# Optimization experiments

Hardware: AMD Instinct MI355X
Metric: run time of the kernel (lower is better)

The kernel has to match this reference:

```python
import jax, jax.numpy as jnp
import numpy as np

B, N, M, C = 8, 76725, 32, 12  # N = 9 anchors x (80^2+40^2+20^2+10^2+5^2) for a 640x640 image, P3-P7
IMG = 640.0


def setup_inputs() -> dict:
    key = jax.random.key(0)
    ks = jax.random.split(key, 7)
    # logits biased toward prior_prob~0.01 like the head's bias init
    cls_logits = jax.random.normal(ks[0], (B, N, C), jnp.float32) - 4.0
    box_deltas = 0.1 * jax.random.normal(ks[1], (B, N, 4), jnp.float32)
    # plausible anchors: random centers in image, sizes 16..256
    a_xy = jax.random.uniform(ks[2], (N, 2), jnp.float32) * IMG
    a_wh = 16.0 + jax.random.uniform(ks[3], (N, 2), jnp.float32) * 240.0
    anchors = jnp.concatenate([a_xy - 0.5 * a_wh, a_xy + 0.5 * a_wh], axis=-1)
    # padded ground truth: M boxes per image, all valid
    g_xy = jax.random.uniform(ks[4], (B, M, 2), jnp.float32) * (IMG - 96.0)
    g_wh = 16.0 + jax.random.uniform(ks[5], (B, M, 2), jnp.float32) * 80.0
    gt_boxes = jnp.concatenate([g_xy, g_xy + g_wh], axis=-1)
    gt_labels = jax.random.randint(ks[6], (B, M), 0, C)
    gt_valid = jnp.ones((B, M), dtype=bool)
    return {"cls_logits": cls_logits, "box_deltas": box_deltas, "anchors": anchors,
            "gt_boxes": gt_boxes, "gt_labels": gt_labels, "gt_valid": gt_valid}


def _box_iou(anchors, gt_boxes):
    # anchors [N,4], gt_boxes [B,M,4] -> [B,N,M]
    ax1, ay1, ax2, ay2 = (anchors[:, i] for i in range(4))
    gx1, gy1, gx2, gy2 = (gt_boxes[..., i] for i in range(4))
    iw = jnp.clip(jnp.minimum(ax2[None, :, None], gx2[:, None, :])
                  - jnp.maximum(ax1[None, :, None], gx1[:, None, :]), 0.0)
    ih = jnp.clip(jnp.minimum(ay2[None, :, None], gy2[:, None, :])
                  - jnp.maximum(ay1[None, :, None], gy1[:, None, :]), 0.0)
    inter = iw * ih
    area_a = (ax2 - ax1) * (ay2 - ay1)            # [N]
    area_g = (gx2 - gx1) * (gy2 - gy1)            # [B,M]
    union = area_a[None, :, None] + area_g[:, None, :] - inter
    return inter / union


def _encode_boxes(anchors, matched):
    aw = anchors[:, 2] - anchors[:, 0]
    ah = anchors[:, 3] - anchors[:, 1]
    acx = anchors[:, 0] + 0.5 * aw
    acy = anchors[:, 1] + 0.5 * ah
    gw = matched[..., 2] - matched[..., 0]
    gh = matched[..., 3] - matched[..., 1]
    gcx = matched[..., 0] + 0.5 * gw
    gcy = matched[..., 1] + 0.5 * gh
    return jnp.stack([(gcx - acx) / aw, (gcy - acy) / ah,
                      jnp.log(gw / aw), jnp.log(gh / ah)], axis=-1)


def reference(cls_logits, box_deltas, anchors, gt_boxes, gt_labels, gt_valid):
    # --- anchor assignment (box_iou + max over GT) ---
    ious = _box_iou(anchors, gt_boxes)                       # [B,N,M]
    ious = jnp.where(gt_valid[:, None, :], ious, -1.0)
    iou_max = ious.max(axis=-1)                              # [B,N]
    idx = ious.argmax(axis=-1)                               # [B,N]
    pos = iou_max >= 0.5
    valid = pos | (iou_max < 0.4)                            # non-ignore anchors
    matched = jnp.take_along_axis(
        gt_boxes, jnp.broadcast_to(idx[:, :, None], (B, N, 4)), axis=1)  # [B,N,4]
    mlab = jnp.take_along_axis(gt_labels, idx, axis=1)       # [B,N]
    f32 = cls_logits.dtype
    cls_t = jax.nn.one_hot(mlab, C, dtype=f32) * pos[..., None].astype(f32)
    # --- sigmoid focal loss (alpha=0.25, gamma=2), mean over non-ignored elements ---
    p = jax.nn.sigmoid(cls_logits)
    ce = -(cls_t * jax.nn.log_sigmoid(cls_logits)
           + (1.0 - cls_t) * jax.nn.log_sigmoid(-cls_logits))
    pt = cls_t * p + (1.0 - cls_t) * (1.0 - p)
    alpha_t = cls_t * 0.25 + (1.0 - cls_t) * 0.75
    focal = alpha_t * (1.0 - pt) ** 2 * ce                   # [B,N,C]
    vw = valid.astype(f32)
    cls_loss = jnp.sum(focal * vw[..., None]) / jnp.maximum(jnp.sum(vw) * C, 1.0)
    # --- smooth L1 (beta=1) on positives, mean over selected elements ---
    box_t = _encode_boxes(anchors, matched)                  # [B,N,4]
    d = jnp.abs(box_deltas - box_t)
    sl1 = jnp.where(d < 1.0, 0.5 * d * d, d - 0.5)
    pw = pos.astype(f32)
    box_loss = jnp.sum(sl1 * pw[..., None]) / jnp.maximum(jnp.sum(pw) * 4.0, 1.0)
    return cls_loss + box_loss
```

## Files before the change

kernel.cpp:

```cpp
#include <hip/hip_runtime.h>
#include <math.h>

#define NB 8
#define NA 76725
#define NM 32
#define NC 12
#define BLK 256
#define GX  128
#define NBLOCKS (GX * NB)
#define NSLOTS 64
#define QUOTA (NBLOCKS / NSLOTS)


__global__ __launch_bounds__(BLK) void retina_fused(
    const float* __restrict__ cls_logits,
    const float* __restrict__ box_deltas,
    const float* __restrict__ anchors,
    const float* __restrict__ gt_boxes,
    const int* __restrict__ gt_labels,
    char* __restrict__ ws,
    unsigned int* __restrict__ cnt2,
    float* __restrict__ out)
{
    __shared__ float4 s_gt[NM];
    __shared__ float  s_area[NM];
    __shared__ int    s_lab[NM];
    __shared__ int    s_islast;

    const int b   = blockIdx.y;
    const int tid = threadIdx.x;

    if (tid < NM) {
        float4 g = ((const float4*)gt_boxes)[b * NM + tid];
        s_gt[tid]   = g;
        s_area[tid] = (g.z - g.x) * (g.w - g.y);
        s_lab[tid]  = gt_labels[b * NM + tid];
    }
    __syncthreads();

    float fsum = 0.0f;
    float ssum = 0.0f;
    int   vcnt = 0;
    int   pcnt = 0;

    for (int n0 = blockIdx.x * BLK; n0 < NA; n0 += GX * BLK) {
        const int n = n0 + tid;
        if (n >= NA) break;

        const float4 a = ((const float4*)anchors)[n];
        const float4* cl = (const float4*)(cls_logits + ((size_t)b * NA + n) * NC);
        const float4 c0 = cl[0], c1 = cl[1], c2 = cl[2];

        const float area_a = (a.z - a.x) * (a.w - a.y);

        float b_inter, b_uni;
        int   bidx = 0;
        {
            const float4 g = s_gt[0];
            const float iw = fmaxf(fminf(a.z, g.z) - fmaxf(a.x, g.x), 0.0f);
            const float ih = fmaxf(fminf(a.w, g.w) - fmaxf(a.y, g.y), 0.0f);
            b_inter = iw * ih;
            b_uni   = (area_a + s_area[0]) - b_inter;
        }
        #pragma unroll
        for (int m = 1; m < NM; ++m) {
            const float4 g = s_gt[m];
            const float iw = fmaxf(fminf(a.z, g.z) - fmaxf(a.x, g.x), 0.0f);
            const float ih = fmaxf(fminf(a.w, g.w) - fmaxf(a.y, g.y), 0.0f);
            const float inter = iw * ih;
            const float uni   = (area_a + s_area[m]) - inter;
            const bool gt = inter * b_uni > b_inter * uni;
            b_inter = gt ? inter : b_inter;
            b_uni   = gt ? uni   : b_uni;
            bidx    = gt ? m     : bidx;
        }

        const bool pos   = (b_inter >= 0.5f * b_uni);
        const bool valid = pos || (b_inter < 0.4f * b_uni);
        vcnt += valid ? 1 : 0;
        pcnt += pos ? 1 : 0;

        if (valid) {
            const int lab = pos ? s_lab[bidx] : -1;
            float x[NC];
            x[0]=c0.x; x[1]=c0.y; x[2]=c0.z; x[3]=c0.w;
            x[4]=c1.x; x[5]=c1.y; x[6]=c1.z; x[7]=c1.w;
            x[8]=c2.x; x[9]=c2.y; x[10]=c2.z; x[11]=c2.w;
            #pragma unroll
            for (int c = 0; c < NC; ++c) {
                const float xx = x[c];
                const float ax = fabsf(xx);
                const float e  = __expf(-ax);
                const float t  = 1.0f + e;
                const float l1pe = __logf(t);
                const float u  = __builtin_amdgcn_rcpf(t);
                const float v  = e * u;
                const bool xpos = (xx >= 0.0f);
                const float sp_mx = l1pe + fmaxf(-xx, 0.0f);
                const float sp_px = l1pe + fmaxf(xx, 0.0f);
                const bool tgt = (c == lab);
                const float q = tgt ? (xpos ? v : u) : (xpos ? u : v);
                const float s = tgt ? sp_mx : sp_px;
                const float al = tgt ? 0.25f : 0.75f;
                fsum += al * q * q * s;
            }
        }

        if (pos) {
            const float4 g = s_gt[bidx];
            const float aw  = a.z - a.x;
            const float ah  = a.w - a.y;
            const float r_aw = __builtin_amdgcn_rcpf(aw);
            const float r_ah = __builtin_amdgcn_rcpf(ah);
            const float acx = a.x + 0.5f * aw;
            const float acy = a.y + 0.5f * ah;
            const float gw  = g.z - g.x;
            const float gh  = g.w - g.y;
            const float gcx = g.x + 0.5f * gw;
            const float gcy = g.y + 0.5f * gh;
            const float t0 = (gcx - acx) * r_aw;
            const float t1 = (gcy - acy) * r_ah;
            const float t2 = __logf(gw * r_aw);
            const float t3 = __logf(gh * r_ah);
            const float4 d4 =
                ((const float4*)box_deltas)[(size_t)b * NA + n];
            float d;
            d = fabsf(d4.x - t0); ssum += (d < 1.0f) ? 0.5f * d * d : d - 0.5f;
            d = fabsf(d4.y - t1); ssum += (d < 1.0f) ? 0.5f * d * d : d - 0.5f;
            d = fabsf(d4.z - t2); ssum += (d < 1.0f) ? 0.5f * d * d : d - 0.5f;
            d = fabsf(d4.w - t3); ssum += (d < 1.0f) ? 0.5f * d * d : d - 0.5f;
        }
    }

    float4 v = make_float4(fsum, ssum, (float)vcnt, (float)pcnt);
    #pragma unroll
    for (int off = 32; off > 0; off >>= 1) {
        v.x += __shfl_down(v.x, off);
        v.y += __shfl_down(v.y, off);
        v.z += __shfl_down(v.z, off);
        v.w += __shfl_down(v.w, off);
    }
    __shared__ float4 s_red[BLK / 64];
    const int wave = tid >> 6;
    const int lane = tid & 63;
    if (lane == 0) s_red[wave] = v;
    __syncthreads();

    if (tid == 0) {
        float4 t = s_red[0];
        #pragma unroll
        for (int w = 1; w < BLK / 64; ++w) {
            t.x += s_red[w].x; t.y += s_red[w].y;
            t.z += s_red[w].z; t.w += s_red[w].w;
        }
        const int flat = blockIdx.y * GX + blockIdx.x;
        const int slot = flat & (NSLOTS - 1);
        double* acc = (double*)(ws + (size_t)slot * 64);
        atomicAdd(&acc[0], (double)t.x);
        atomicAdd(&acc[1], (double)t.y);
        atomicAdd(&acc[2], (double)t.z);
        atomicAdd(&acc[3], (double)t.w);
        __threadfence();
        unsigned int* slot_cnt = (unsigned int*)(ws + (size_t)slot * 64 + 32);
        const unsigned int old = atomicAdd(slot_cnt, 1u);
        int islast = 0;
        if (old == QUOTA - 1) {
            __threadfence();
            const unsigned int o2 = atomicAdd(cnt2, 1u);
            islast = (o2 == NSLOTS - 1) ? 1 : 0;
        }
        s_islast = islast;
    }
    __syncthreads();

    if (s_islast) {
        __threadfence();
        __shared__ double s_acc[NSLOTS][4];
        if (tid < NSLOTS) {
            const double* acc = (const double*)(ws + (size_t)tid * 64);
            #pragma unroll
            for (int j = 0; j < 4; ++j)
                s_acc[tid][j] = __hip_atomic_load(&acc[j], __ATOMIC_RELAXED,
                                                  __HIP_MEMORY_SCOPE_AGENT);
        }
        __syncthreads();
        if (tid == 0) {
            double fs = 0.0, ss = 0.0, vc = 0.0, pc = 0.0;
            for (int k = 0; k < NSLOTS; ++k) {
                fs += s_acc[k][0]; ss += s_acc[k][1];
                vc += s_acc[k][2]; pc += s_acc[k][3];
            }
            const double cls_loss = fs / fmax(vc * (double)NC, 1.0);
            const double box_loss = ss / fmax(pc * 4.0, 1.0);
            out[0] = (float)(cls_loss + box_loss);
        }
    }
}

extern "C" void kernel_launch(void* const* d_in, const int* in_sizes, int n_in,
                              void* d_out, int out_size, void* d_ws, size_t ws_size,
                              hipStream_t stream) {
    const float* cls_logits = (const float*)d_in[0];
    const float* box_deltas = (const float*)d_in[1];
    const float* anchors    = (const float*)d_in[2];
    const float* gt_boxes   = (const float*)d_in[3];
    const int*   gt_labels  = (const int*)d_in[4];
    float* out = (float*)d_out;

    char* ws = (char*)d_ws;
    unsigned int* cnt2 = (unsigned int*)(ws + (size_t)NSLOTS * 64);

    hipMemsetAsync(d_ws, 0, (size_t)NSLOTS * 64 + 4, stream);
    dim3 grid(GX, NB);
    retina_fused<<<grid, BLK, 0, stream>>>(
        cls_logits, box_deltas, anchors, gt_boxes, gt_labels,
        ws, cnt2, out);
}
```

Measured before the change: 124.8 us.

## Compute focal loss unconditionally and split IoU argmax into parallel groups

The focal loss for all 12 classes is now computed without a branch, treating every class as a negative. For positive anchors, the target class term is fixed up by reloading that single logit and swapping the negative term for the positive one. The 32-box IoU argmax is split into four independent chains of 8 and then merged in a small tree, which shortens the serial dependency chain and removes divergence around the valid branch. The cost is a transcendental pass on ignored anchors, an extra scattered global load for positives, and tie-breaking and rounding that may differ slightly from before.

```diff
diff --git a/kernel.cpp b/kernel.cpp
--- a/kernel.cpp
+++ b/kernel.cpp
@@ -53,60 +53,91 @@
 
         const float area_a = (a.z - a.x) * (a.w - a.y);
 
-        float b_inter, b_uni;
-        int   bidx = 0;
-        {
-            const float4 g = s_gt[0];
-            const float iw = fmaxf(fminf(a.z, g.z) - fmaxf(a.x, g.x), 0.0f);
-            const float ih = fmaxf(fminf(a.w, g.w) - fmaxf(a.y, g.y), 0.0f);
-            b_inter = iw * ih;
-            b_uni   = (area_a + s_area[0]) - b_inter;
-        }
+        float x[NC];
+        x[0]=c0.x; x[1]=c0.y; x[2]=c0.z; x[3]=c0.w;
+        x[4]=c1.x; x[5]=c1.y; x[6]=c1.z; x[7]=c1.w;
+        x[8]=c2.x; x[9]=c2.y; x[10]=c2.z; x[11]=c2.w;
+        float fall = 0.0f;
         #pragma unroll
-        for (int m = 1; m < NM; ++m) {
-            const float4 g = s_gt[m];
-            const float iw = fmaxf(fminf(a.z, g.z) - fmaxf(a.x, g.x), 0.0f);
-            const float ih = fmaxf(fminf(a.w, g.w) - fmaxf(a.y, g.y), 0.0f);
-            const float inter = iw * ih;
-            const float uni   = (area_a + s_area[m]) - inter;
-            const bool gt = inter * b_uni > b_inter * uni;
-            b_inter = gt ? inter : b_inter;
-            b_uni   = gt ? uni   : b_uni;
-            bidx    = gt ? m     : bidx;
-        }
+        for (int c = 0; c < NC; ++c) {
+            const float xx = x[c];
+            const float ax = fabsf(xx);
+            const float e  = __expf(-ax);
+            const float t  = 1.0f + e;
+            const float l1pe = __logf(t);
+            const float u  = __builtin_amdgcn_rcpf(t);
+            const float pm = e * u;
+            const float p  = (xx >= 0.0f) ? u : pm;
+            const float sp = l1pe + fmaxf(xx, 0.0f);
+            fall += p * p * sp;
+        }
+
+        float gi[4], gu[4];
+        int   gx[4];
+        #pragma unroll
+        for (int grp = 0; grp < 4; ++grp) {
+            const int base = grp << 3;
+            float bi_, bu_;
+            int   bx_ = base;
+            {
+                const float4 g = s_gt[base];
+                const float iw = fmaxf(fminf(a.z, g.z) - fmaxf(a.x, g.x), 0.0f);
+                const float ih = fmaxf(fminf(a.w, g.w) - fmaxf(a.y, g.y), 0.0f);
+                bi_ = iw * ih;
+                bu_ = (area_a + s_area[base]) - bi_;
+            }
+            #pragma unroll
+            for (int j = 1; j < 8; ++j) {
+                const int m = base + j;
+                const float4 g = s_gt[m];
+                const float iw = fmaxf(fminf(a.z, g.z) - fmaxf(a.x, g.x), 0.0f);
+                const float ih = fmaxf(fminf(a.w, g.w) - fmaxf(a.y, g.y), 0.0f);
+                const float inter = iw * ih;
+                const float uni   = (area_a + s_area[m]) - inter;
+                const bool gt = inter * bu_ > bi_ * uni;
+                bi_ = gt ? inter : bi_;
+                bu_ = gt ? uni   : bu_;
+                bx_ = gt ? m     : bx_;
+            }
+            gi[grp] = bi_; gu[grp] = bu_; gx[grp] = bx_;
+        }
+        const bool m01 = gi[1] * gu[0] > gi[0] * gu[1];
+        const float i01 = m01 ? gi[1] : gi[0];
+        const float u01 = m01 ? gu[1] : gu[0];
+        const int   x01 = m01 ? gx[1] : gx[0];
+        const bool m23 = gi[3] * gu[2] > gi[2] * gu[3];
+        const float i23 = m23 ? gi[3] : gi[2];
+        const float u23 = m23 ? gu[3] : gu[2];
+        const int   x23 = m23 ? gx[3] : gx[2];
+        const bool mf = i23 * u01 > i01 * u23;
+        const float b_inter = mf ? i23 : i01;
+        const float b_uni   = mf ? u23 : u01;
+        const int   bidx    = mf ? x23 : x01;
 
         const bool pos   = (b_inter >= 0.5f * b_uni);
         const bool valid = pos || (b_inter < 0.4f * b_uni);
         vcnt += valid ? 1 : 0;
         pcnt += pos ? 1 : 0;
 
-        if (valid) {
-            const int lab = pos ? s_lab[bidx] : -1;
-            float x[NC];
-            x[0]=c0.x; x[1]=c0.y; x[2]=c0.z; x[3]=c0.w;
-            x[4]=c1.x; x[5]=c1.y; x[6]=c1.z; x[7]=c1.w;
-            x[8]=c2.x; x[9]=c2.y; x[10]=c2.z; x[11]=c2.w;
-            #pragma unroll
-            for (int c = 0; c < NC; ++c) {
-                const float xx = x[c];
-                const float ax = fabsf(xx);
-                const float e  = __expf(-ax);
-                const float t  = 1.0f + e;
-                const float l1pe = __logf(t);
-                const float u  = __builtin_amdgcn_rcpf(t);
-                const float v  = e * u;
-                const bool xpos = (xx >= 0.0f);
-                const float sp_mx = l1pe + fmaxf(-xx, 0.0f);
-                const float sp_px = l1pe + fmaxf(xx, 0.0f);
-                const bool tgt = (c == lab);
-                const float q = tgt ? (xpos ? v : u) : (xpos ? u : v);
-                const float s = tgt ? sp_mx : sp_px;
-                const float al = tgt ? 0.25f : 0.75f;
-                fsum += al * q * q * s;
-            }
-        }
+        fsum += valid ? 0.75f * fall : 0.0f;
 
         if (pos) {
+            const int lab = s_lab[bidx];
+            const float xl = cls_logits[((size_t)b * NA + n) * NC + lab];
+            const float ax = fabsf(xl);
+            const float e  = __expf(-ax);
+            const float t  = 1.0f + e;
+            const float l1pe = __logf(t);
+            const float u  = __builtin_amdgcn_rcpf(t);
+            const float pm = e * u;
+            const float p  = (xl >= 0.0f) ? u : pm;
+            const float omp = (xl >= 0.0f) ? pm : u;
+            const float sp_px = l1pe + fmaxf(xl, 0.0f);
+            const float sp_mx = l1pe + fmaxf(-xl, 0.0f);
+            const float tgt = 0.25f * omp * omp * sp_mx;
+            const float nt  = 0.75f * p * p * sp_px;
+            fsum += tgt - nt;
+
             const float4 g = s_gt[bidx];
             const float aw  = a.z - a.x;
             const float ah  = a.w - a.y;
```

New measurement: 126.0 us. About the same (+1.0%).

## Launch one block per anchor tile and compute focal loss as all-negative plus target correction

Applied to the files above, without the earlier changes.

Replaces the grid-stride loop with one 256-anchor tile per block (300 blocks per image, 60 accumulator slots), so each thread handles one anchor. The focal loss is now computed unconditionally for every class as if negative, and a single-class correction for the labelled class is added only on positive anchors. This removes the per-class target select and the divergent valid branch. The shared-memory GT staging and its barrier are dropped in favour of direct global reads, and the IoU thresholds are rewritten as cross-multiplied comparisons on intersection and area sum. The cost is a larger grid with more blocks doing atomics, plus an extra scattered logit load on positives.

```diff
diff --git a/kernel.cpp b/kernel.cpp
--- a/kernel.cpp
+++ b/kernel.cpp
@@ -6,9 +6,9 @@
 #define NM 32
 #define NC 12
 #define BLK 256
-#define GX  128
-#define NBLOCKS (GX * NB)
-#define NSLOTS 64
+#define NBLK_X ((NA + BLK - 1) / BLK)
+#define NBLOCKS (NBLK_X * NB)
+#define NSLOTS 60
 #define QUOTA (NBLOCKS / NSLOTS)
 
 
@@ -22,92 +22,94 @@
     unsigned int* __restrict__ cnt2,
     float* __restrict__ out)
 {
-    __shared__ float4 s_gt[NM];
-    __shared__ float  s_area[NM];
-    __shared__ int    s_lab[NM];
     __shared__ int    s_islast;
+    __shared__ float4 s_red[BLK / 64];
+    __shared__ double s_acc[NSLOTS][4];
 
     const int b   = blockIdx.y;
     const int tid = threadIdx.x;
-
-    if (tid < NM) {
-        float4 g = ((const float4*)gt_boxes)[b * NM + tid];
-        s_gt[tid]   = g;
-        s_area[tid] = (g.z - g.x) * (g.w - g.y);
-        s_lab[tid]  = gt_labels[b * NM + tid];
-    }
-    __syncthreads();
+    const int n   = blockIdx.x * BLK + tid;
+    const bool live = (n < NA);
+
+    const float4* __restrict__ gtb =
+        (const float4*)(gt_boxes + (size_t)b * NM * 4);
 
     float fsum = 0.0f;
     float ssum = 0.0f;
     int   vcnt = 0;
     int   pcnt = 0;
 
-    for (int n0 = blockIdx.x * BLK; n0 < NA; n0 += GX * BLK) {
-        const int n = n0 + tid;
-        if (n >= NA) break;
-
+    if (live) {
         const float4 a = ((const float4*)anchors)[n];
         const float4* cl = (const float4*)(cls_logits + ((size_t)b * NA + n) * NC);
         const float4 c0 = cl[0], c1 = cl[1], c2 = cl[2];
-
         const float area_a = (a.z - a.x) * (a.w - a.y);
 
-        float b_inter, b_uni;
+        float xs[NC];
+        xs[0]=c0.x; xs[1]=c0.y; xs[2]=c0.z; xs[3]=c0.w;
+        xs[4]=c1.x; xs[5]=c1.y; xs[6]=c1.z; xs[7]=c1.w;
+        xs[8]=c2.x; xs[9]=c2.y; xs[10]=c2.z; xs[11]=c2.w;
+        float fall = 0.0f;
+        #pragma unroll
+        for (int c = 0; c < NC; ++c) {
+            const float xx = xs[c];
+            const float ax = fabsf(xx);
+            const float e  = __expf(-ax);
+            const float t  = 1.0f + e;
+            const float l1pe = __logf(t);
+            const float u  = __builtin_amdgcn_rcpf(t);
+            const float pm = e * u;
+            const float p  = (xx >= 0.0f) ? u : pm;
+            const float sp = l1pe + fmaxf(xx, 0.0f);
+            fall += p * p * sp;
+        }
+
+        float b_i, b_S;
         int   bidx = 0;
         {
-            const float4 g = s_gt[0];
+            const float4 g = gtb[0];
             const float iw = fmaxf(fminf(a.z, g.z) - fmaxf(a.x, g.x), 0.0f);
             const float ih = fmaxf(fminf(a.w, g.w) - fmaxf(a.y, g.y), 0.0f);
-            b_inter = iw * ih;
-            b_uni   = (area_a + s_area[0]) - b_inter;
+            b_i = iw * ih;
+            b_S = area_a + (g.z - g.x) * (g.w - g.y);
         }
         #pragma unroll
         for (int m = 1; m < NM; ++m) {
-            const float4 g = s_gt[m];
+            const float4 g = gtb[m];
             const float iw = fmaxf(fminf(a.z, g.z) - fmaxf(a.x, g.x), 0.0f);
             const float ih = fmaxf(fminf(a.w, g.w) - fmaxf(a.y, g.y), 0.0f);
             const float inter = iw * ih;
-            const float uni   = (area_a + s_area[m]) - inter;
-            const bool gt = inter * b_uni > b_inter * uni;
-            b_inter = gt ? inter : b_inter;
-            b_uni   = gt ? uni   : b_uni;
-            bidx    = gt ? m     : bidx;
-        }
-
-        const bool pos   = (b_inter >= 0.5f * b_uni);
-        const bool valid = pos || (b_inter < 0.4f * b_uni);
-        vcnt += valid ? 1 : 0;
-        pcnt += pos ? 1 : 0;
-
-        if (valid) {
-            const int lab = pos ? s_lab[bidx] : -1;
-            float x[NC];
-            x[0]=c0.x; x[1]=c0.y; x[2]=c0.z; x[3]=c0.w;
-            x[4]=c1.x; x[5]=c1.y; x[6]=c1.z; x[7]=c1.w;
-            x[8]=c2.x; x[9]=c2.y; x[10]=c2.z; x[11]=c2.w;
-            #pragma unroll
-            for (int c = 0; c < NC; ++c) {
-                const float xx = x[c];
-                const float ax = fabsf(xx);
-                const float e  = __expf(-ax);
-                const float t  = 1.0f + e;
-                const float l1pe = __logf(t);
-                const float u  = __builtin_amdgcn_rcpf(t);
-                const float v  = e * u;
-                const bool xpos = (xx >= 0.0f);
-                const float sp_mx = l1pe + fmaxf(-xx, 0.0f);
-                const float sp_px = l1pe + fmaxf(xx, 0.0f);
-                const bool tgt = (c == lab);
-                const float q = tgt ? (xpos ? v : u) : (xpos ? u : v);
-                const float s = tgt ? sp_mx : sp_px;
-                const float al = tgt ? 0.25f : 0.75f;
-                fsum += al * q * q * s;
-            }
-        }
+            const float S = area_a + (g.z - g.x) * (g.w - g.y);
+            const bool gt = inter * b_S > b_i * S;
+            b_i  = gt ? inter : b_i;
+            b_S  = gt ? S     : b_S;
+            bidx = gt ? m     : bidx;
+        }
+
+        const bool pos   = (3.0f * b_i >= b_S);
+        const bool valid = pos || (7.0f * b_i < 2.0f * b_S);
+        vcnt = valid ? 1 : 0;
+        pcnt = pos ? 1 : 0;
+
+        fsum = valid ? 0.75f * fall : 0.0f;
 
         if (pos) {
-            const float4 g = s_gt[bidx];
+            const int lab = gt_labels[b * NM + bidx];
+            const float xl = xs[0] * 0.0f +
+                cls_logits[((size_t)b * NA + n) * NC + lab];
+            const float ax = fabsf(xl);
+            const float e  = __expf(-ax);
+            const float t  = 1.0f + e;
+            const float l1pe = __logf(t);
+            const float u  = __builtin_amdgcn_rcpf(t);
+            const float pm = e * u;
+            const float p  = (xl >= 0.0f) ? u : pm;
+            const float omp = (xl >= 0.0f) ? pm : u;
+            const float sp_px = l1pe + fmaxf(xl, 0.0f);
+            const float sp_mx = l1pe + fmaxf(-xl, 0.0f);
+            fsum += 0.25f * omp * omp * sp_mx - 0.75f * p * p * sp_px;
+
+            const float4 g = gtb[bidx];
             const float aw  = a.z - a.x;
             const float ah  = a.w - a.y;
             const float r_aw = __builtin_amdgcn_rcpf(aw);
@@ -122,8 +124,7 @@
             const float t1 = (gcy - acy) * r_ah;
             const float t2 = __logf(gw * r_aw);
             const float t3 = __logf(gh * r_ah);
-            const float4 d4 =
-                ((const float4*)box_deltas)[(size_t)b * NA + n];
+            const float4 d4 = ((const float4*)box_deltas)[(size_t)b * NA + n];
             float d;
             d = fabsf(d4.x - t0); ssum += (d < 1.0f) ? 0.5f * d * d : d - 0.5f;
             d = fabsf(d4.y - t1); ssum += (d < 1.0f) ? 0.5f * d * d : d - 0.5f;
@@ -140,7 +141,6 @@
         v.z += __shfl_down(v.z, off);
         v.w += __shfl_down(v.w, off);
     }
-    __shared__ float4 s_red[BLK / 64];
     const int wave = tid >> 6;
     const int lane = tid & 63;
     if (lane == 0) s_red[wave] = v;
@@ -153,8 +153,8 @@
             t.x += s_red[w].x; t.y += s_red[w].y;
             t.z += s_red[w].z; t.w += s_red[w].w;
         }
-        const int flat = blockIdx.y * GX + blockIdx.x;
-        const int slot = flat & (NSLOTS - 1);
+        const int flat = blockIdx.y * NBLK_X + blockIdx.x;
+        const int slot = flat % NSLOTS;
         double* acc = (double*)(ws + (size_t)slot * 64);
         atomicAdd(&acc[0], (double)t.x);
         atomicAdd(&acc[1], (double)t.y);
@@ -175,7 +175,6 @@
 
     if (s_islast) {
         __threadfence();
-        __shared__ double s_acc[NSLOTS][4];
         if (tid < NSLOTS) {
             const double* acc = (const double*)(ws + (size_t)tid * 64);
             #pragma unroll
@@ -211,7 +210,7 @@
     unsigned int* cnt2 = (unsigned int*)(ws + (size_t)NSLOTS * 64);
 
     hipMemsetAsync(d_ws, 0, (size_t)NSLOTS * 64 + 4, stream);
-    dim3 grid(GX, NB);
+    dim3 grid(NBLK_X, NB);
     retina_fused<<<grid, BLK, 0, stream>>>(
         cls_logits, box_deltas, anchors, gt_boxes, gt_labels,
         ws, cnt2, out);
```

Result: slower. 148.5 us (+19.0%).
